# Kernel tuning notes

Measured on AMD Instinct MI355X. Metric: run time of the kernel, lower is better.

The kernel has to match this reference:

```python
import jax, jax.numpy as jnp
import numpy as np

N = 100000
E = 3200000
D = 128
EPS = 1e-5


def setup_inputs() -> dict:
    key = jax.random.key(0)
    ks = jax.random.split(key, 9)
    h = jax.random.normal(ks[0], (N, D), dtype=jnp.float32)
    src = jax.random.randint(ks[1], (E,), 0, N, dtype=jnp.int64)
    dst = jax.random.randint(ks[2], (E,), 0, N, dtype=jnp.int64)
    s = 1.0 / np.sqrt(D)
    W_self = jax.random.uniform(ks[3], (D, D), jnp.float32, -s, s)
    W_neigh = jax.random.uniform(ks[4], (D, D), jnp.float32, -s, s)
    b = jax.random.uniform(ks[5], (D,), jnp.float32, -s, s)
    gamma = jnp.ones((D,), jnp.float32)
    beta = jnp.zeros((D,), jnp.float32)
    return {"h": h, "src": src, "dst": dst, "W_self": W_self,
            "W_neigh": W_neigh, "b": b, "gamma": gamma, "beta": beta}


def reference(h, src, dst, W_self, W_neigh, b, gamma, beta):
    # --- SAGEConv, mean aggregator (dropout p=0 -> identity) ---
    # gather source features along edges, segment-mean into destination nodes
    neigh_sum = jax.ops.segment_sum(h[src], dst, num_segments=N)      # [N, D]
    deg = jax.ops.segment_sum(jnp.ones((E,), h.dtype), dst, num_segments=N)
    neigh = neigh_sum / jnp.maximum(deg, 1.0)[:, None]                # [N, D]
    rst = h @ W_self + neigh @ W_neigh + b                            # [N, D]
    rst = jax.nn.relu(rst)                                            # activation
    # --- BatchNorm1d (training-mode batch statistics) ---
    mean = jnp.mean(rst, axis=0)
    var = jnp.var(rst, axis=0)
    rst = (rst - mean) * jax.lax.rsqrt(var + EPS) * gamma + beta
    # --- residual (in_feats == out_feats) ---
    return h + rst
```

## Files before the change

kernel.cpp:

```cpp
#include <hip/hip_runtime.h>

#define DCAP 2432
#define NBMAX 1600
#define PB 256
#define GB 1024

typedef __attribute__((ext_vector_type(2))) float f32x2;
typedef __attribute__((ext_vector_type(4))) float f32x4;
typedef __attribute__((ext_vector_type(8))) short bf16x8;

__device__ __forceinline__ unsigned short f2bf(float f) {
  union { float f; unsigned u; } c; c.f = f;
  unsigned u = c.u;
  unsigned r = u + 0x7FFFu + ((u >> 16) & 1u);
  return (unsigned short)(r >> 16);
}
__device__ __forceinline__ float bf2f(unsigned short s) {
  union { unsigned u; float f; } c; c.u = ((unsigned)s) << 16;
  return c.f;
}

__global__ void k_convert(const float* __restrict__ h, unsigned short* __restrict__ X,
                          unsigned* __restrict__ X8, int nnodes) {
  int stride = gridDim.x * blockDim.x;
  int total = nnodes * 32;
  for (int i = blockIdx.x * blockDim.x + threadIdx.x; i < total; i += stride) {
    int n = i >> 5, c = i & 31;
    float4 v = *(const float4*)(h + (long)n * 128 + c * 4);
    ushort4 o;
    o.x = f2bf(v.x); o.y = f2bf(v.y); o.z = f2bf(v.z); o.w = f2bf(v.w);
    *(ushort4*)(X + (long)n * 256 + c * 4) = o;
    int p8 = __builtin_amdgcn_cvt_pk_fp8_f32(v.x, v.y, 0, false);
    p8 = __builtin_amdgcn_cvt_pk_fp8_f32(v.z, v.w, p8, true);
    X8[(long)n * 32 + c] = (unsigned)p8;
  }
}

__global__ __launch_bounds__(1024) void k_cnt(const int* __restrict__ dst,
                                              int* __restrict__ cnt_mat, int E, int NB) {
  __shared__ int cnt[NBMAX];
  int t = threadIdx.x;
  int chunk = (E + gridDim.x - 1) / gridDim.x;
  int e0 = blockIdx.x * chunk;
  int e1 = e0 + chunk; if (e1 > E) e1 = E;
  for (int i = t; i < NB; i += 1024) cnt[i] = 0;
  __syncthreads();
  for (int e = e0 + t; e < e1; e += 1024)
    atomicAdd(&cnt[dst[e] >> 6], 1);
  __syncthreads();
  for (int i = t; i < NB; i += 1024)
    cnt_mat[blockIdx.x * NBMAX + i] = cnt[i];
}

__global__ __launch_bounds__(PB) void k_ofs(const int* __restrict__ cnt_mat,
                                            int* __restrict__ ofs_mat,
                                            int* __restrict__ gcur, int NB) {
  __shared__ int l[PB];
  int b = blockIdx.x, t = threadIdx.x;
  int v = cnt_mat[t * NBMAX + b];
  l[t] = v;
  __syncthreads();
  for (int off = 1; off < PB; off <<= 1) {
    int add = (t >= off) ? l[t - off] : 0;
    __syncthreads();
    l[t] += add;
    __syncthreads();
  }
  int ex = l[t] - v;
  ofs_mat[t * NBMAX + b] = ex;
  if (t == PB - 1) gcur[b] = l[t];
}

__global__ __launch_bounds__(1024) void k_scat(const int* __restrict__ dst,
                                               const int* __restrict__ src,
                                               const int* __restrict__ ofs_mat,
                                               unsigned* __restrict__ buck, int E, int NB) {
  __shared__ int cur[NBMAX];
  int t = threadIdx.x;
  int chunk = (E + gridDim.x - 1) / gridDim.x;
  int e0 = blockIdx.x * chunk;
  int e1 = e0 + chunk; if (e1 > E) e1 = E;
  for (int i = t; i < NB; i += 1024) cur[i] = ofs_mat[blockIdx.x * NBMAX + i];
  __syncthreads();
  for (int e = e0 + t; e < e1; e += 1024) {
    int d = dst[e];
    int b = d >> 6;
    int p = atomicAdd(&cur[b], 1);
    if (p < DCAP)
      buck[(long)b * DCAP + p] = ((unsigned)src[e] << 6) | (unsigned)(d & 63);
  }
}

__global__ void k_wprep(const float* __restrict__ Ws, const float* __restrict__ Wn,
                        unsigned short* __restrict__ Wt) {
  int i = blockIdx.x * blockDim.x + threadIdx.x;
  if (i >= 128 * 256) return;
  int col = i >> 8, k = i & 255;
  float v = (k < 128) ? Ws[k * 128 + col] : Wn[(k - 128) * 128 + col];
  Wt[col * 256 + k] = f2bf(v);
}

__global__ __launch_bounds__(256) void k_aggb(unsigned short* __restrict__ X,
                                              const unsigned* __restrict__ X8,
                                              const unsigned* __restrict__ buck,
                                              const int* __restrict__ gcur,
                                              int nnodes) {
  __shared__ unsigned eload[DCAP];
  __shared__ unsigned eord[DCAP];
  __shared__ int dcnt[64], dstart[64], dcur[64], sc[64];
  int t = threadIdx.x;
  int b = blockIdx.x;
  int cntE = gcur[b]; if (cntE > DCAP) cntE = DCAP;
  if (t < 64) dcnt[t] = 0;
  __syncthreads();
  for (int i = t; i < cntE; i += 256) {
    unsigned p = buck[(long)b * DCAP + i];
    eload[i] = p;
    atomicAdd(&dcnt[p & 63u], 1);
  }
  __syncthreads();
  if (t < 64) sc[t] = dcnt[t];
  __syncthreads();
  for (int off = 1; off < 64; off <<= 1) {
    int v = (t < 64 && t >= off) ? sc[t - off] : 0;
    __syncthreads();
    if (t < 64) sc[t] += v;
    __syncthreads();
  }
  if (t < 64) { int ex = sc[t] - dcnt[t]; dstart[t] = ex; dcur[t] = ex; }
  __syncthreads();
  for (int i = t; i < cntE; i += 256) {
    unsigned p = eload[i];
    int pos = atomicAdd(&dcur[p & 63u], 1);
    eord[pos] = p >> 6;
  }
  __syncthreads();

  int lane = t & 63, w = t >> 6;
  int half = lane >> 5, hl = lane & 31;
  int ndst = nnodes - b * 64; if (ndst > 64) ndst = 64;
  for (int dl = w; dl < ndst; dl += 4) {
    int n = b * 64 + dl;
    int start = dstart[dl], dn = dcnt[dl];
    f32x2 a01[2], a23[2];
#pragma unroll
    for (int u = 0; u < 2; u++) {
      a01[u].x = 0.f; a01[u].y = 0.f;
      a23[u].x = 0.f; a23[u].y = 0.f;
    }
    int i = 0;
    for (; i + 16 <= dn; i += 16) {
      unsigned v[8];
#pragma unroll
      for (int u = 0; u < 8; u++) {
        int e = (int)eord[start + i + 2 * u + half];
        v[u] = X8[(long)e * 32 + hl];
      }
#pragma unroll
      for (int u = 0; u < 8; u++) {
        a01[u & 1] += __builtin_amdgcn_cvt_pk_f32_fp8(v[u], false);
        a23[u & 1] += __builtin_amdgcn_cvt_pk_f32_fp8(v[u], true);
      }
    }
    for (; i + 2 <= dn; i += 2) {
      int e = (int)eord[start + i + half];
      unsigned v = X8[(long)e * 32 + hl];
      a01[0] += __builtin_amdgcn_cvt_pk_f32_fp8(v, false);
      a23[0] += __builtin_amdgcn_cvt_pk_f32_fp8(v, true);
    }
    if (i < dn && half == 0) {
      int e = (int)eord[start + i];
      unsigned v = X8[(long)e * 32 + hl];
      a01[0] += __builtin_amdgcn_cvt_pk_f32_fp8(v, false);
      a23[0] += __builtin_amdgcn_cvt_pk_f32_fp8(v, true);
    }
    float s0 = a01[0].x + a01[1].x;
    float s1 = a01[0].y + a01[1].y;
    float s2 = a23[0].x + a23[1].x;
    float s3 = a23[0].y + a23[1].y;
    s0 += __shfl_down(s0, 32);
    s1 += __shfl_down(s1, 32);
    s2 += __shfl_down(s2, 32);
    s3 += __shfl_down(s3, 32);
    if (half == 0) {
      float scl = 1.0f / fmaxf((float)dn, 1.0f);
      ushort4 o;
      o.x = f2bf(s0 * scl); o.y = f2bf(s1 * scl);
      o.z = f2bf(s2 * scl); o.w = f2bf(s3 * scl);
      *(ushort4*)(X + (long)n * 256 + 128 + hl * 4) = o;
    }
  }
}

__global__ __launch_bounds__(256) void k_gemm(const unsigned short* __restrict__ X,
                                              const unsigned short* __restrict__ Wt,
                                              const float* __restrict__ bias,
                                              unsigned short* __restrict__ rst8,
                                              float* __restrict__ psum,
                                              float* __restrict__ psq,
                                              int nnodes, int ntiles) {
  int t = threadIdx.x;
  int w = t >> 6, lane = t & 63;
  int m = lane & 15, q = lane >> 4;
  int col0 = w * 32 + m;
  int col1 = col0 + 16;
  bf16x8 b0[8], b1[8];
#pragma unroll
  for (int ks = 0; ks < 8; ks++) {
    b0[ks] = *(const bf16x8*)(Wt + col0 * 256 + q * 8 + ks * 32);
    b1[ks] = *(const bf16x8*)(Wt + col1 * 256 + q * 8 + ks * 32);
  }
  float bv0 = bias[col0], bv1 = bias[col1];
  float s0 = 0.f, sq0 = 0.f, s1 = 0.f, sq1 = 0.f;

  for (int tb = blockIdx.x; tb < ntiles; tb += GB) {
    int rowm = tb * 16 + m; if (rowm >= nnodes) rowm = nnodes - 1;
    const unsigned short* xp = X + (long)rowm * 256 + q * 8;
    bf16x8 a[8];
#pragma unroll
    for (int ks = 0; ks < 8; ks++) a[ks] = *(const bf16x8*)(xp + ks * 32);
    f32x4 acc0 = {0.f, 0.f, 0.f, 0.f};
    f32x4 acc1 = {0.f, 0.f, 0.f, 0.f};
#pragma unroll
    for (int ks = 0; ks < 8; ks++) {
      acc0 = __builtin_amdgcn_mfma_f32_16x16x32_bf16(a[ks], b0[ks], acc0, 0, 0, 0);
      acc1 = __builtin_amdgcn_mfma_f32_16x16x32_bf16(a[ks], b1[ks], acc1, 0, 0, 0);
    }
#pragma unroll
    for (int r = 0; r < 4; r++) {
      int row = tb * 16 + q * 4 + r;
      if (row < nnodes) {
        float v0 = acc0[r] + bv0; v0 = v0 > 0.f ? v0 : 0.f;
        float v1 = acc1[r] + bv1; v1 = v1 > 0.f ? v1 : 0.f;
        rst8[(long)row * 128 + col0] = f2bf(v0);
        rst8[(long)row * 128 + col1] = f2bf(v1);
        s0 += v0; sq0 += v0 * v0;
        s1 += v1; sq1 += v1 * v1;
      }
    }
  }
  s0 += __shfl_down(s0, 32);  s0 += __shfl_down(s0, 16);
  sq0 += __shfl_down(sq0, 32); sq0 += __shfl_down(sq0, 16);
  s1 += __shfl_down(s1, 32);  s1 += __shfl_down(s1, 16);
  sq1 += __shfl_down(sq1, 32); sq1 += __shfl_down(sq1, 16);
  if (lane < 16) {
    long o = (long)blockIdx.x * 128;
    psum[o + col0] = s0;  psum[o + col1] = s1;
    psq[o + col0] = sq0;  psq[o + col1] = sq1;
  }
}

__global__ __launch_bounds__(1024) void k_redstat(const float* __restrict__ psum,
                                                  const float* __restrict__ psq,
                                                  const float* __restrict__ gamma,
                                                  const float* __restrict__ beta,
                                                  float* __restrict__ scale,
                                                  float* __restrict__ shift, float Nf) {
  __shared__ float l1[1024], l2[1024];
  int t = threadIdx.x;
  int col = t & 127, sl = t >> 7;
  float s = 0.f, s2 = 0.f;
  for (int b = sl; b < GB; b += 8) {
    s += psum[b * 128 + col];
    s2 += psq[b * 128 + col];
  }
  l1[t] = s; l2[t] = s2;
  __syncthreads();
  if (t < 128) {
#pragma unroll
    for (int i = 1; i < 8; i++) { s += l1[t + i * 128]; s2 += l2[t + i * 128]; }
    float mean = s / Nf;
    float var = s2 / Nf - mean * mean;
    float inv = rsqrtf(var + 1e-5f);
    float scv = gamma[t] * inv;
    scale[t] = scv;
    shift[t] = beta[t] - mean * scv;
  }
}

__global__ void k_final(const float* __restrict__ h, float* __restrict__ out,
                        const unsigned short* __restrict__ rst8,
                        const float* __restrict__ scale, const float* __restrict__ shift,
                        int nnodes) {
  __shared__ float sc_s[128], sh_s[128];
  int t = threadIdx.x;
  if (t < 128) { sc_s[t] = scale[t]; sh_s[t] = shift[t]; }
  __syncthreads();
  int stride = gridDim.x * blockDim.x;
  int total = nnodes * 16;
  for (int i = blockIdx.x * blockDim.x + threadIdx.x; i < total; i += stride) {
    int c = i & 15;
    uint4 rv = *(const uint4*)(rst8 + (long)i * 8);
    float4 h0 = *(const float4*)(h + (long)i * 8);
    float4 h1 = *(const float4*)(h + (long)i * 8 + 4);
    float4 sc0 = *(const float4*)(sc_s + c * 8);
    float4 sc1 = *(const float4*)(sc_s + c * 8 + 4);
    float4 sh0 = *(const float4*)(sh_s + c * 8);
    float4 sh1 = *(const float4*)(sh_s + c * 8 + 4);
    float4 o0, o1;
    o0.x = h0.x + bf2f((unsigned short)(rv.x & 0xFFFFu)) * sc0.x + sh0.x;
    o0.y = h0.y + bf2f((unsigned short)(rv.x >> 16)) * sc0.y + sh0.y;
    o0.z = h0.z + bf2f((unsigned short)(rv.y & 0xFFFFu)) * sc0.z + sh0.z;
    o0.w = h0.w + bf2f((unsigned short)(rv.y >> 16)) * sc0.w + sh0.w;
    o1.x = h1.x + bf2f((unsigned short)(rv.z & 0xFFFFu)) * sc1.x + sh1.x;
    o1.y = h1.y + bf2f((unsigned short)(rv.z >> 16)) * sc1.y + sh1.y;
    o1.z = h1.z + bf2f((unsigned short)(rv.w & 0xFFFFu)) * sc1.z + sh1.z;
    o1.w = h1.w + bf2f((unsigned short)(rv.w >> 16)) * sc1.w + sh1.w;
    *(float4*)(out + (long)i * 8) = o0;
    *(float4*)(out + (long)i * 8 + 4) = o1;
  }
}

extern "C" void kernel_launch(void* const* d_in, const int* in_sizes, int n_in,
                              void* d_out, int out_size, void* d_ws, size_t ws_size,
                              hipStream_t stream) {
  const float* h     = (const float*)d_in[0];
  const int*   src   = (const int*)d_in[1];
  const int*   dst   = (const int*)d_in[2];
  const float* Ws    = (const float*)d_in[3];
  const float* Wn    = (const float*)d_in[4];
  const float* bias  = (const float*)d_in[5];
  const float* gamma = (const float*)d_in[6];
  const float* beta  = (const float*)d_in[7];
  float* out = (float*)d_out;

  int nnodes = in_sizes[0] / 128;
  int E = in_sizes[1];
  int NB = (nnodes + 63) >> 6;
  int ntiles = (nnodes + 15) >> 4;

  char* ws = (char*)d_ws;
  size_t off = 0;
  unsigned short* X = (unsigned short*)(ws + off); off += (size_t)nnodes * 256 * 2;
  size_t off_alias = off;
  unsigned* X8 = (unsigned*)(ws + off);            off += (size_t)nnodes * 128;
  unsigned* buck = (unsigned*)(ws + off);          off += (size_t)NB * DCAP * 4;
  unsigned short* rst8 = (unsigned short*)(ws + off_alias);
  int* gcur = (int*)(ws + off);                    off += NBMAX * 4;
  unsigned short* Wt = (unsigned short*)(ws + off); off += 128 * 256 * 2;
  float* psum = (float*)(ws + off);                off += (size_t)GB * 128 * 4;
  float* psq = (float*)(ws + off);                 off += (size_t)GB * 128 * 4;
  float* scale = (float*)(ws + off);               off += 512;
  float* shift = (float*)(ws + off);               off += 512;
  int* cnt_mat = (int*)(ws + off);                 off += (size_t)PB * NBMAX * 4;
  int* ofs_mat = (int*)(ws + off);                 off += (size_t)PB * NBMAX * 4;

  k_convert<<<4096, 256, 0, stream>>>(h, X, X8, nnodes);
  k_cnt<<<PB, 1024, 0, stream>>>(dst, cnt_mat, E, NB);
  k_ofs<<<NB, PB, 0, stream>>>(cnt_mat, ofs_mat, gcur, NB);
  k_scat<<<PB, 1024, 0, stream>>>(dst, src, ofs_mat, buck, E, NB);
  k_wprep<<<128, 256, 0, stream>>>(Ws, Wn, Wt);
  k_aggb<<<NB, 256, 0, stream>>>(X, X8, buck, gcur, nnodes);
  k_gemm<<<GB, 256, 0, stream>>>(X, Wt, bias, rst8, psum, psq, nnodes, ntiles);
  k_redstat<<<1, 1024, 0, stream>>>(psum, psq, gamma, beta, scale, shift, (float)nnodes);
  k_final<<<4096, 256, 0, stream>>>(h, out, rst8, scale, shift, nnodes);
}
```

Baseline: 356.5 us.

## Fuse convert, count and weight-prep kernels; widen aggregation gathers to 8 bytes

Merges the bf16/fp8 convert, per-bucket edge count and weight transpose into one launch with block-range dispatch, removing two kernel launches and letting the count phase overlap the conversion. Halves the partition count used by counting and scatter. In aggregation it drops the LDS staging copy of bucket entries and reads them directly from global twice. It also has each lane gather 8 fp8 bytes (quarter-row per 16 lanes, 4 edges in flight per wavefront) instead of 4, with a two-step shuffle reduction and 16-byte stores. Fewer partitions lower the per-partition scatter parallelism, and the extra bucket reads add global traffic.

```diff
diff --git a/kernel.cpp b/kernel.cpp
--- a/kernel.cpp
+++ b/kernel.cpp
@@ -2,7 +2,9 @@
 
 #define DCAP 2432
 #define NBMAX 1600
-#define PB 256
+#define PB2 128
+#define CONVB 2048
+#define WPB 128
 #define GB 1024
 
 typedef __attribute__((ext_vector_type(2))) float f32x2;
@@ -20,47 +22,62 @@
   return c.f;
 }
 
-__global__ void k_convert(const float* __restrict__ h, unsigned short* __restrict__ X,
-                          unsigned* __restrict__ X8, int nnodes) {
-  int stride = gridDim.x * blockDim.x;
-  int total = nnodes * 32;
-  for (int i = blockIdx.x * blockDim.x + threadIdx.x; i < total; i += stride) {
-    int n = i >> 5, c = i & 31;
-    float4 v = *(const float4*)(h + (long)n * 128 + c * 4);
-    ushort4 o;
-    o.x = f2bf(v.x); o.y = f2bf(v.y); o.z = f2bf(v.z); o.w = f2bf(v.w);
-    *(ushort4*)(X + (long)n * 256 + c * 4) = o;
-    int p8 = __builtin_amdgcn_cvt_pk_fp8_f32(v.x, v.y, 0, false);
-    p8 = __builtin_amdgcn_cvt_pk_fp8_f32(v.z, v.w, p8, true);
-    X8[(long)n * 32 + c] = (unsigned)p8;
-  }
-}
-
-__global__ __launch_bounds__(1024) void k_cnt(const int* __restrict__ dst,
-                                              int* __restrict__ cnt_mat, int E, int NB) {
+__global__ __launch_bounds__(256) void k_pre(const float* __restrict__ h,
+                                             unsigned short* __restrict__ X,
+                                             unsigned* __restrict__ X8,
+                                             const int* __restrict__ dst,
+                                             int* __restrict__ cnt_mat,
+                                             const float* __restrict__ Ws,
+                                             const float* __restrict__ Wn,
+                                             unsigned short* __restrict__ Wt,
+                                             int nnodes, int E, int NB) {
   __shared__ int cnt[NBMAX];
   int t = threadIdx.x;
-  int chunk = (E + gridDim.x - 1) / gridDim.x;
-  int e0 = blockIdx.x * chunk;
-  int e1 = e0 + chunk; if (e1 > E) e1 = E;
-  for (int i = t; i < NB; i += 1024) cnt[i] = 0;
-  __syncthreads();
-  for (int e = e0 + t; e < e1; e += 1024)
-    atomicAdd(&cnt[dst[e] >> 6], 1);
-  __syncthreads();
-  for (int i = t; i < NB; i += 1024)
-    cnt_mat[blockIdx.x * NBMAX + i] = cnt[i];
-}
-
-__global__ __launch_bounds__(PB) void k_ofs(const int* __restrict__ cnt_mat,
-                                            int* __restrict__ ofs_mat,
-                                            int* __restrict__ gcur, int NB) {
-  __shared__ int l[PB];
+  int bid = blockIdx.x;
+  if (bid < CONVB) {
+    int stride = CONVB * 256;
+    int total = nnodes * 32;
+    for (int i = bid * 256 + t; i < total; i += stride) {
+      int n = i >> 5, c = i & 31;
+      float4 v = *(const float4*)(h + (long)n * 128 + c * 4);
+      ushort4 o;
+      o.x = f2bf(v.x); o.y = f2bf(v.y); o.z = f2bf(v.z); o.w = f2bf(v.w);
+      *(ushort4*)(X + (long)n * 256 + c * 4) = o;
+      int p8 = __builtin_amdgcn_cvt_pk_fp8_f32(v.x, v.y, 0, false);
+      p8 = __builtin_amdgcn_cvt_pk_fp8_f32(v.z, v.w, p8, true);
+      X8[(long)n * 32 + c] = (unsigned)p8;
+    }
+  } else if (bid < CONVB + PB2) {
+    int bb = bid - CONVB;
+    int chunk = (E + PB2 - 1) / PB2;
+    int e0 = bb * chunk;
+    int e1 = e0 + chunk; if (e1 > E) e1 = E;
+    for (int i = t; i < NB; i += 256) cnt[i] = 0;
+    __syncthreads();
+    for (int e = e0 + t; e < e1; e += 256)
+      atomicAdd(&cnt[dst[e] >> 6], 1);
+    __syncthreads();
+    for (int i = t; i < NB; i += 256)
+      cnt_mat[bb * NBMAX + i] = cnt[i];
+  } else {
+    int i = (bid - CONVB - PB2) * 256 + t;
+    if (i < 128 * 256) {
+      int col = i >> 8, k = i & 255;
+      float v = (k < 128) ? Ws[k * 128 + col] : Wn[(k - 128) * 128 + col];
+      Wt[col * 256 + k] = f2bf(v);
+    }
+  }
+}
+
+__global__ __launch_bounds__(PB2) void k_ofs(const int* __restrict__ cnt_mat,
+                                             int* __restrict__ ofs_mat,
+                                             int* __restrict__ gcur, int NB) {
+  __shared__ int l[PB2];
   int b = blockIdx.x, t = threadIdx.x;
   int v = cnt_mat[t * NBMAX + b];
   l[t] = v;
   __syncthreads();
-  for (int off = 1; off < PB; off <<= 1) {
+  for (int off = 1; off < PB2; off <<= 1) {
     int add = (t >= off) ? l[t - off] : 0;
     __syncthreads();
     l[t] += add;
@@ -68,7 +85,7 @@
   }
   int ex = l[t] - v;
   ofs_mat[t * NBMAX + b] = ex;
-  if (t == PB - 1) gcur[b] = l[t];
+  if (t == PB2 - 1) gcur[b] = l[t];
 }
 
 __global__ __launch_bounds__(1024) void k_scat(const int* __restrict__ dst,
@@ -77,7 +94,7 @@
                                                unsigned* __restrict__ buck, int E, int NB) {
   __shared__ int cur[NBMAX];
   int t = threadIdx.x;
-  int chunk = (E + gridDim.x - 1) / gridDim.x;
+  int chunk = (E + PB2 - 1) / PB2;
   int e0 = blockIdx.x * chunk;
   int e1 = e0 + chunk; if (e1 > E) e1 = E;
   for (int i = t; i < NB; i += 1024) cur[i] = ofs_mat[blockIdx.x * NBMAX + i];
@@ -91,21 +108,11 @@
   }
 }
 
-__global__ void k_wprep(const float* __restrict__ Ws, const float* __restrict__ Wn,
-                        unsigned short* __restrict__ Wt) {
-  int i = blockIdx.x * blockDim.x + threadIdx.x;
-  if (i >= 128 * 256) return;
-  int col = i >> 8, k = i & 255;
-  float v = (k < 128) ? Ws[k * 128 + col] : Wn[(k - 128) * 128 + col];
-  Wt[col * 256 + k] = f2bf(v);
-}
-
 __global__ __launch_bounds__(256) void k_aggb(unsigned short* __restrict__ X,
-                                              const unsigned* __restrict__ X8,
+                                              const unsigned char* __restrict__ X8,
                                               const unsigned* __restrict__ buck,
                                               const int* __restrict__ gcur,
                                               int nnodes) {
-  __shared__ unsigned eload[DCAP];
   __shared__ unsigned eord[DCAP];
   __shared__ int dcnt[64], dstart[64], dcur[64], sc[64];
   int t = threadIdx.x;
@@ -113,11 +120,9 @@
   int cntE = gcur[b]; if (cntE > DCAP) cntE = DCAP;
   if (t < 64) dcnt[t] = 0;
   __syncthreads();
-  for (int i = t; i < cntE; i += 256) {
-    unsigned p = buck[(long)b * DCAP + i];
-    eload[i] = p;
-    atomicAdd(&dcnt[p & 63u], 1);
-  }
+  const unsigned* bp = buck + (long)b * DCAP;
+  for (int i = t; i < cntE; i += 256)
+    atomicAdd(&dcnt[bp[i] & 63u], 1);
   __syncthreads();
   if (t < 64) sc[t] = dcnt[t];
   __syncthreads();
@@ -130,64 +135,74 @@
   if (t < 64) { int ex = sc[t] - dcnt[t]; dstart[t] = ex; dcur[t] = ex; }
   __syncthreads();
   for (int i = t; i < cntE; i += 256) {
-    unsigned p = eload[i];
+    unsigned p = bp[i];
     int pos = atomicAdd(&dcur[p & 63u], 1);
     eord[pos] = p >> 6;
   }
   __syncthreads();
 
   int lane = t & 63, w = t >> 6;
-  int half = lane >> 5, hl = lane & 31;
+  int qt = lane >> 4, ql = lane & 15;
   int ndst = nnodes - b * 64; if (ndst > 64) ndst = 64;
   for (int dl = w; dl < ndst; dl += 4) {
-    int n = b * 64 + dl;
     int start = dstart[dl], dn = dcnt[dl];
-    f32x2 a01[2], a23[2];
-#pragma unroll
-    for (int u = 0; u < 2; u++) {
-      a01[u].x = 0.f; a01[u].y = 0.f;
-      a23[u].x = 0.f; a23[u].y = 0.f;
-    }
+    f32x2 acc[2][4];
+#pragma unroll
+    for (int u = 0; u < 2; u++)
+#pragma unroll
+      for (int j = 0; j < 4; j++) { acc[u][j].x = 0.f; acc[u][j].y = 0.f; }
     int i = 0;
     for (; i + 16 <= dn; i += 16) {
-      unsigned v[8];
-#pragma unroll
-      for (int u = 0; u < 8; u++) {
-        int e = (int)eord[start + i + 2 * u + half];
-        v[u] = X8[(long)e * 32 + hl];
+      uint2 v[4];
+#pragma unroll
+      for (int u = 0; u < 4; u++) {
+        unsigned e = eord[start + i + u * 4 + qt];
+        v[u] = *(const uint2*)(X8 + e * 128u + ql * 8u);
       }
 #pragma unroll
-      for (int u = 0; u < 8; u++) {
-        a01[u & 1] += __builtin_amdgcn_cvt_pk_f32_fp8(v[u], false);
-        a23[u & 1] += __builtin_amdgcn_cvt_pk_f32_fp8(v[u], true);
+      for (int u = 0; u < 4; u++) {
+        acc[u & 1][0] += __builtin_amdgcn_cvt_pk_f32_fp8(v[u].x, false);
+        acc[u & 1][1] += __builtin_amdgcn_cvt_pk_f32_fp8(v[u].x, true);
+        acc[u & 1][2] += __builtin_amdgcn_cvt_pk_f32_fp8(v[u].y, false);
+        acc[u & 1][3] += __builtin_amdgcn_cvt_pk_f32_fp8(v[u].y, true);
       }
     }
-    for (; i + 2 <= dn; i += 2) {
-      int e = (int)eord[start + i + half];
-      unsigned v = X8[(long)e * 32 + hl];
-      a01[0] += __builtin_amdgcn_cvt_pk_f32_fp8(v, false);
-      a23[0] += __builtin_amdgcn_cvt_pk_f32_fp8(v, true);
-    }
-    if (i < dn && half == 0) {
-      int e = (int)eord[start + i];
-      unsigned v = X8[(long)e * 32 + hl];
-      a01[0] += __builtin_amdgcn_cvt_pk_f32_fp8(v, false);
-      a23[0] += __builtin_amdgcn_cvt_pk_f32_fp8(v, true);
-    }
-    float s0 = a01[0].x + a01[1].x;
-    float s1 = a01[0].y + a01[1].y;
-    float s2 = a23[0].x + a23[1].x;
-    float s3 = a23[0].y + a23[1].y;
-    s0 += __shfl_down(s0, 32);
-    s1 += __shfl_down(s1, 32);
-    s2 += __shfl_down(s2, 32);
-    s3 += __shfl_down(s3, 32);
-    if (half == 0) {
+    for (; i + 4 <= dn; i += 4) {
+      unsigned e = eord[start + i + qt];
+      uint2 v = *(const uint2*)(X8 + e * 128u + ql * 8u);
+      acc[0][0] += __builtin_amdgcn_cvt_pk_f32_fp8(v.x, false);
+      acc[0][1] += __builtin_amdgcn_cvt_pk_f32_fp8(v.x, true);
+      acc[0][2] += __builtin_amdgcn_cvt_pk_f32_fp8(v.y, false);
+      acc[0][3] += __builtin_amdgcn_cvt_pk_f32_fp8(v.y, true);
+    }
+    int rem = dn - i;
+    if (qt < rem) {
+      unsigned e = eord[start + i + qt];
+      uint2 v = *(const uint2*)(X8 + e * 128u + ql * 8u);
+      acc[1][0] += __builtin_amdgcn_cvt_pk_f32_fp8(v.x, false);
+      acc[1][1] += __builtin_amdgcn_cvt_pk_f32_fp8(v.x, true);
+      acc[1][2] += __builtin_amdgcn_cvt_pk_f32_fp8(v.y, false);
+      acc[1][3] += __builtin_amdgcn_cvt_pk_f32_fp8(v.y, true);
+    }
+    float s[8];
+#pragma unroll
+    for (int j = 0; j < 4; j++) {
+      s[2 * j] = acc[0][j].x + acc[1][j].x;
+      s[2 * j + 1] = acc[0][j].y + acc[1][j].y;
+    }
+#pragma unroll
+    for (int j = 0; j < 8; j++) {
+      s[j] += __shfl_down(s[j], 32);
+      s[j] += __shfl_down(s[j], 16);
+    }
+    if (qt == 0) {
       float scl = 1.0f / fmaxf((float)dn, 1.0f);
-      ushort4 o;
-      o.x = f2bf(s0 * scl); o.y = f2bf(s1 * scl);
-      o.z = f2bf(s2 * scl); o.w = f2bf(s3 * scl);
-      *(ushort4*)(X + (long)n * 256 + 128 + hl * 4) = o;
+      uint4 o;
+      o.x = (unsigned)f2bf(s[0] * scl) | ((unsigned)f2bf(s[1] * scl) << 16);
+      o.y = (unsigned)f2bf(s[2] * scl) | ((unsigned)f2bf(s[3] * scl) << 16);
+      o.z = (unsigned)f2bf(s[4] * scl) | ((unsigned)f2bf(s[5] * scl) << 16);
+      o.w = (unsigned)f2bf(s[6] * scl) | ((unsigned)f2bf(s[7] * scl) << 16);
+      *(uint4*)(X + (long)(b * 64 + dl) * 256 + 128 + ql * 8) = o;
     }
   }
 }
@@ -342,15 +357,14 @@
   float* psq = (float*)(ws + off);                 off += (size_t)GB * 128 * 4;
   float* scale = (float*)(ws + off);               off += 512;
   float* shift = (float*)(ws + off);               off += 512;
-  int* cnt_mat = (int*)(ws + off);                 off += (size_t)PB * NBMAX * 4;
-  int* ofs_mat = (int*)(ws + off);                 off += (size_t)PB * NBMAX * 4;
-
-  k_convert<<<4096, 256, 0, stream>>>(h, X, X8, nnodes);
-  k_cnt<<<PB, 1024, 0, stream>>>(dst, cnt_mat, E, NB);
-  k_ofs<<<NB, PB, 0, stream>>>(cnt_mat, ofs_mat, gcur, NB);
-  k_scat<<<PB, 1024, 0, stream>>>(dst, src, ofs_mat, buck, E, NB);
-  k_wprep<<<128, 256, 0, stream>>>(Ws, Wn, Wt);
-  k_aggb<<<NB, 256, 0, stream>>>(X, X8, buck, gcur, nnodes);
+  int* cnt_mat = (int*)(ws + off);                 off += (size_t)PB2 * NBMAX * 4;
+  int* ofs_mat = (int*)(ws + off);                 off += (size_t)PB2 * NBMAX * 4;
+
+  k_pre<<<CONVB + PB2 + WPB, 256, 0, stream>>>(h, X, X8, dst, cnt_mat, Ws, Wn, Wt,
+                                               nnodes, E, NB);
+  k_ofs<<<NB, PB2, 0, stream>>>(cnt_mat, ofs_mat, gcur, NB);
+  k_scat<<<PB2, 1024, 0, stream>>>(dst, src, ofs_mat, buck, E, NB);
+  k_aggb<<<NB, 256, 0, stream>>>(X, (const unsigned char*)X8, buck, gcur, nnodes);
   k_gemm<<<GB, 256, 0, stream>>>(X, Wt, bias, rst8, psum, psq, nnodes, ntiles);
   k_redstat<<<1, 1024, 0, stream>>>(psum, psq, gamma, beta, scale, shift, (float)nnodes);
   k_final<<<4096, 256, 0, stream>>>(h, out, rst8, scale, shift, nnodes);
```

Result: slower. 399.8 us (+12.2%).
